# Kernel optimization log

Measured on AMD Instinct MI355X. Metric: run time of the kernel, lower is better.

## Reference

```python
import jax, jax.numpy as jnp
import numpy as np

N, F_IN, F_OUT = 8192, 1024, 512
ALPHA = 0.2   # LeakyReLU negative slope
C = 0.5       # RWR restart constant (hardcoded in original forward)


def setup_inputs() -> dict:
    key = jax.random.key(0)
    ks = jax.random.split(key, 9)
    x = jax.random.normal(ks[0], (N, F_IN), jnp.float32)
    adj = jax.random.normal(ks[1], (N, N), jnp.float32)  # additive attention bias
    adj_ad = jax.random.randint(ks[2], (N, N), 0, 20, jnp.int32)
    seq_W = jax.random.normal(ks[3], (F_OUT, F_IN), jnp.float32) / np.float32(np.sqrt(F_IN))
    f1_w = jax.random.normal(ks[4], (F_OUT,), jnp.float32) / np.float32(np.sqrt(F_OUT))
    f1_b = jax.random.normal(ks[5], (1,), jnp.float32)
    f2_w = jax.random.normal(ks[6], (F_OUT,), jnp.float32) / np.float32(np.sqrt(F_OUT))
    f2_b = jax.random.normal(ks[7], (1,), jnp.float32)
    bias = jnp.zeros((F_OUT,), jnp.float32)
    return {"x": x, "adj": adj, "adj_ad": adj_ad, "seq_W": seq_W,
            "f1_w": f1_w, "f1_b": f1_b, "f2_w": f2_w, "f2_b": f2_b, "bias": bias}


def _rwr(adj_ad):
    # Per-node random-walk-with-restart on a star graph over the selected
    # neighbors: solve (I - c*W) r = e0 where W is the (k_i+1)x(k_i+1) star
    # adjacency. Closed form of the per-node torch.inverse loop:
    #   r0 = 1 / (1 - c^2 k),  r_j = c / (1 - c^2 k)   (abs taken in original)
    # If (I - c*W) is singular the original falls back to rw_left = I - c*W,
    # giving r0 = 1, r_j = -c.
    k = jnp.sum((adj_ad > 1) & (adj_ad < 4), axis=1).astype(jnp.float32)  # [N]
    denom = 1.0 - (C * C) * k
    singular = denom == 0.0
    safe = jnp.where(singular, 1.0, denom)
    ri0 = jnp.where(singular, 1.0, jnp.abs(1.0 / safe))
    rin = jnp.where(singular, C, jnp.abs(C / safe))
    return jnp.stack([ri0, rin], axis=-1)  # [N, 2]: (center value, per-neighbor value)


def reference(x, adj, adj_ad, seq_W, f1_w, f1_b, f2_w, f2_b, bias):
    # conv1d(kernel=1) == linear: [N, F_IN] @ [F_IN, F_OUT]
    seq_fts = x @ seq_W.T                                  # [N, F_OUT]
    f1 = seq_fts @ f1_w + f1_b                             # [N]
    f2 = seq_fts @ f2_w + f2_b                             # [N]
    logits = f1[:, None] + f2[None, :]                     # [N, N]
    pre = jnp.where(logits > 0, logits, ALPHA * logits) + adj
    coefs = jax.nn.softmax(pre, axis=1)                    # dropout = identity (eval)
    h_prime = coefs @ seq_fts + bias                       # [N, F_OUT]
    h_prime = jax.nn.elu(h_prime)                          # concat=True
    ri = _rwr(adj_ad)
    return h_prime, ri
```

## Files before the change

kernel.cpp:

```cpp
#include <hip/hip_runtime.h>

#define NROWS 8192
#define FIN 1024
#define FOUT 512

typedef __attribute__((ext_vector_type(8))) short short8;
typedef __attribute__((ext_vector_type(4))) float f32x4;
typedef __attribute__((ext_vector_type(4))) unsigned short us4;

static __device__ __forceinline__ unsigned short f2bf(float f) {
  unsigned int u = __float_as_uint(f);
  u += 0x7fffu + ((u >> 16) & 1u);
  return (unsigned short)(u >> 16);
}
static __device__ __forceinline__ float bf2f(unsigned short h) {
  return __uint_as_float(((unsigned int)h) << 16);
}
static __device__ __forceinline__ void load_lds16(const void* g, void* l) {
  __builtin_amdgcn_global_load_lds((const __attribute__((address_space(1))) void*)g,
                                   (__attribute__((address_space(3))) void*)l, 16, 0, 0);
}

static __device__ __forceinline__ float dpp16_max(float x) {
  int t;
  t = __builtin_amdgcn_update_dpp(0, __float_as_int(x), 0xB1, 0xf, 0xf, true);
  x = fmaxf(x, __int_as_float(t));
  t = __builtin_amdgcn_update_dpp(0, __float_as_int(x), 0x4E, 0xf, 0xf, true);
  x = fmaxf(x, __int_as_float(t));
  t = __builtin_amdgcn_update_dpp(0, __float_as_int(x), 0x124, 0xf, 0xf, true);
  x = fmaxf(x, __int_as_float(t));
  t = __builtin_amdgcn_update_dpp(0, __float_as_int(x), 0x128, 0xf, 0xf, true);
  x = fmaxf(x, __int_as_float(t));
  return x;
}
static __device__ __forceinline__ float dpp16_add(float x) {
  int t;
  t = __builtin_amdgcn_update_dpp(0, __float_as_int(x), 0xB1, 0xf, 0xf, true);
  x += __int_as_float(t);
  t = __builtin_amdgcn_update_dpp(0, __float_as_int(x), 0x4E, 0xf, 0xf, true);
  x += __int_as_float(t);
  t = __builtin_amdgcn_update_dpp(0, __float_as_int(x), 0x124, 0xf, 0xf, true);
  x += __int_as_float(t);
  t = __builtin_amdgcn_update_dpp(0, __float_as_int(x), 0x128, 0xf, 0xf, true);
  x += __int_as_float(t);
  return x;
}

__global__ void k_split(const float* __restrict__ x, const float* __restrict__ w,
                        unsigned short* __restrict__ hi, unsigned short* __restrict__ lo) {
  long long base = ((long long)blockIdx.x * blockDim.x + threadIdx.x) * 4;
  const long long NX = (long long)NROWS * FIN;
  const float* src = (base < NX) ? (x + base) : (w + (base - NX));
  float4 v = *(const float4*)src;
  unsigned short h0 = f2bf(v.x), h1 = f2bf(v.y), h2 = f2bf(v.z), h3 = f2bf(v.w);
  us4 hv = {h0, h1, h2, h3};
  us4 lv = {f2bf(v.x - bf2f(h0)), f2bf(v.y - bf2f(h1)),
            f2bf(v.z - bf2f(h2)), f2bf(v.w - bf2f(h3))};
  *(us4*)(hi + base) = hv;
  *(us4*)(lo + base) = lv;
}

__global__ __launch_bounds__(256) void k_gemm1(const unsigned short* __restrict__ ah,
                                               const unsigned short* __restrict__ al,
                                               float* __restrict__ c) {
  __shared__ unsigned short sAh[128 * 32], sAl[128 * 32], sBh[64 * 32], sBl[64 * 32];
  const int tid = threadIdx.x;
  const int w = tid >> 6, l = tid & 63;
  const int bm = blockIdx.x >> 3, bn = blockIdx.x & 7;
  const int i0 = bm * 128, n0 = bn * 64;
  const unsigned short* bhp = ah + (long long)NROWS * FIN;
  const unsigned short* blp = al + (long long)NROWS * FIN;
  const int m_off = (w & 1) * 64, n_off = (w >> 1) * 32;
  const int lrow = l >> 2, lch = (l & 3) * 8;
  f32x4 acc[4][2] = {};
  for (int k0 = 0; k0 < FIN; k0 += 32) {
    __syncthreads();
    {
      int rA0 = w * 32, rA1 = w * 32 + 16, rB = w * 16;
      long long ga0 = (long long)(i0 + rA0 + lrow) * FIN + k0 + lch;
      long long ga1 = (long long)(i0 + rA1 + lrow) * FIN + k0 + lch;
      long long gb = (long long)(n0 + rB + lrow) * FIN + k0 + lch;
      load_lds16(ah + ga0, &sAh[rA0 * 32]);
      load_lds16(ah + ga1, &sAh[rA1 * 32]);
      load_lds16(al + ga0, &sAl[rA0 * 32]);
      load_lds16(al + ga1, &sAl[rA1 * 32]);
      load_lds16(bhp + gb, &sBh[rB * 32]);
      load_lds16(blp + gb, &sBl[rB * 32]);
    }
    __syncthreads();
    short8 a_h[4], a_l[4], b_h[2], b_l[2];
#pragma unroll
    for (int mi = 0; mi < 4; ++mi) {
      int off = (m_off + mi * 16 + (l & 15)) * 32 + (l >> 4) * 8;
      a_h[mi] = *(const short8*)&sAh[off];
      a_l[mi] = *(const short8*)&sAl[off];
    }
#pragma unroll
    for (int ni = 0; ni < 2; ++ni) {
      int off = (n_off + ni * 16 + (l & 15)) * 32 + (l >> 4) * 8;
      b_h[ni] = *(const short8*)&sBh[off];
      b_l[ni] = *(const short8*)&sBl[off];
    }
#pragma unroll
    for (int mi = 0; mi < 4; ++mi)
#pragma unroll
      for (int ni = 0; ni < 2; ++ni) {
        acc[mi][ni] = __builtin_amdgcn_mfma_f32_16x16x32_bf16(a_h[mi], b_h[ni], acc[mi][ni], 0, 0, 0);
        acc[mi][ni] = __builtin_amdgcn_mfma_f32_16x16x32_bf16(a_h[mi], b_l[ni], acc[mi][ni], 0, 0, 0);
        acc[mi][ni] = __builtin_amdgcn_mfma_f32_16x16x32_bf16(a_l[mi], b_h[ni], acc[mi][ni], 0, 0, 0);
      }
  }
#pragma unroll
  for (int mi = 0; mi < 4; ++mi)
#pragma unroll
    for (int ni = 0; ni < 2; ++ni)
#pragma unroll
      for (int rg = 0; rg < 4; ++rg) {
        int row = i0 + m_off + mi * 16 + (l >> 4) * 4 + rg;
        int col = n0 + n_off + ni * 16 + (l & 15);
        c[(long long)row * FOUT + col] = acc[mi][ni][rg];
      }
}

__global__ void k_f1f2(const float* __restrict__ sf, const float* __restrict__ f1w,
                       const float* __restrict__ f1b, const float* __restrict__ f2w,
                       const float* __restrict__ f2b, float* __restrict__ f1,
                       float* __restrict__ f2) {
  int w = threadIdx.x >> 6, l = threadIdx.x & 63;
  int i = blockIdx.x * 4 + w;
  const float* row = sf + (long long)i * FOUT;
  float4 v0 = *(const float4*)(row + l * 8);
  float4 v1 = *(const float4*)(row + l * 8 + 4);
  float4 a0 = *(const float4*)(f1w + l * 8);
  float4 a1 = *(const float4*)(f1w + l * 8 + 4);
  float4 b0 = *(const float4*)(f2w + l * 8);
  float4 b1 = *(const float4*)(f2w + l * 8 + 4);
  float s1 = v0.x * a0.x + v0.y * a0.y + v0.z * a0.z + v0.w * a0.w +
             v1.x * a1.x + v1.y * a1.y + v1.z * a1.z + v1.w * a1.w;
  float s2 = v0.x * b0.x + v0.y * b0.y + v0.z * b0.z + v0.w * b0.w +
             v1.x * b1.x + v1.y * b1.y + v1.z * b1.z + v1.w * b1.w;
#pragma unroll
  for (int m = 1; m < 64; m <<= 1) {
    s1 += __shfl_xor(s1, m, 64);
    s2 += __shfl_xor(s2, m, 64);
  }
  if (l == 0) {
    f1[i] = s1 + f1b[0];
    f2[i] = s2 + f2b[0];
  }
}

__global__ __launch_bounds__(256) void k_pack(const float* __restrict__ sf,
                                              unsigned short* __restrict__ vtp) {
  __shared__ unsigned short tile[32][33];
  const int t = threadIdx.x;
  const int k0 = blockIdx.x * 32;
  const int n0 = blockIdx.y * 32;
  {
    int kk = t >> 3, nq = (t & 7) * 4;
    float4 v = *(const float4*)(sf + (long long)(k0 + kk) * FOUT + n0 + nq);
    tile[kk][nq] = f2bf(v.x);
    tile[kk][nq + 1] = f2bf(v.y);
    tile[kk][nq + 2] = f2bf(v.z);
    tile[kk][nq + 3] = f2bf(v.w);
  }
  __syncthreads();
  int nt_loc = t >> 7, tt = t & 127;
  int lane = tt >> 1, jh = (tt & 1) * 4;
  int n_loc = nt_loc * 16 + (lane & 15);
  int k_loc = (lane >> 4) * 8 + jh;
  us4 u = {tile[k_loc][n_loc], tile[k_loc + 1][n_loc], tile[k_loc + 2][n_loc],
           tile[k_loc + 3][n_loc]};
  long long kt = blockIdx.x;
  long long nt = (long long)blockIdx.y * 2 + nt_loc;
  *(us4*)(vtp + ((kt * 32 + nt) * 64 + lane) * 8 + jh) = u;
}

__global__ __launch_bounds__(512) void k_flashp(const float* __restrict__ adj,
                                                const float* __restrict__ f1,
                                                const float* __restrict__ f2,
                                                const unsigned short* __restrict__ vtp,
                                                float* __restrict__ pacc,
                                                float* __restrict__ pstats) {
  __shared__ short p_sh[2][2][4][64][8];
  __shared__ float alpha_sh[2][32];
  const int tid = threadIdx.x, l = tid & 63, w = tid >> 6;
  const int rloc = tid >> 4, c16 = tid & 15;
  const int part = (blockIdx.x >> 2) & 1;
  const int rb = ((blockIdx.x >> 3) << 2) | (blockIdx.x & 3);
  const int r0 = rb * 32;
  const int jbase = part * 4096;
  const long long arow = (long long)(r0 + rloc) * NROWS;
  const float f1r = f1[r0 + rloc];
  const int nt_base = w * 4;
  const int mi_p = rloc >> 4;
  const int ks_p = c16 >> 2;
  const int lp = (rloc & 15) | ((c16 & 3) << 4);
  float m = -3.0e38f, lsum = 0.f;
  f32x4 acc[2][4] = {};
  float4 a0 = *(const float4*)(adj + arow + jbase + c16 * 8);
  float4 a1 = *(const float4*)(adj + arow + jbase + c16 * 8 + 4);
  float4 f20 = *(const float4*)(f2 + jbase + c16 * 8);
  float4 f21 = *(const float4*)(f2 + jbase + c16 * 8 + 4);
  for (int t = 0; t < 32; ++t) {
    const int j0 = jbase + t * 128;
    const int buf = t & 1;
    short8 vb[4][4];
    {
      const unsigned short* bb =
          vtp + (((long long)(j0 >> 5) * 32 + nt_base) * 64 + l) * 8;
#pragma unroll
      for (int ks = 0; ks < 4; ++ks)
#pragma unroll
        for (int ni = 0; ni < 4; ++ni)
          vb[ks][ni] = *(const short8*)(bb + ks * 16384 + ni * 512);
    }
    float z, p0, p1, p2, p3, p4, p5, p6, p7;
    z = f1r + f20.x; p0 = (z > 0.f ? z : 0.2f * z) + a0.x;
    z = f1r + f20.y; p1 = (z > 0.f ? z : 0.2f * z) + a0.y;
    z = f1r + f20.z; p2 = (z > 0.f ? z : 0.2f * z) + a0.z;
    z = f1r + f20.w; p3 = (z > 0.f ? z : 0.2f * z) + a0.w;
    z = f1r + f21.x; p4 = (z > 0.f ? z : 0.2f * z) + a1.x;
    z = f1r + f21.y; p5 = (z > 0.f ? z : 0.2f * z) + a1.y;
    z = f1r + f21.z; p6 = (z > 0.f ? z : 0.2f * z) + a1.z;
    z = f1r + f21.w; p7 = (z > 0.f ? z : 0.2f * z) + a1.w;
    float mt = fmaxf(fmaxf(fmaxf(p0, p1), fmaxf(p2, p3)), fmaxf(fmaxf(p4, p5), fmaxf(p6, p7)));
    mt = dpp16_max(mt);
    float m_new = fmaxf(m, mt);
    float al = __expf(m - m_new);
    p0 = __expf(p0 - m_new); p1 = __expf(p1 - m_new);
    p2 = __expf(p2 - m_new); p3 = __expf(p3 - m_new);
    p4 = __expf(p4 - m_new); p5 = __expf(p5 - m_new);
    p6 = __expf(p6 - m_new); p7 = __expf(p7 - m_new);
    float ps = p0 + p1 + p2 + p3 + p4 + p5 + p6 + p7;
    ps = dpp16_add(ps);
    lsum = lsum * al + ps;
    m = m_new;
    if (c16 == 0) alpha_sh[buf][rloc] = al;
    short8 pv;
    pv[0] = (short)f2bf(p0); pv[1] = (short)f2bf(p1);
    pv[2] = (short)f2bf(p2); pv[3] = (short)f2bf(p3);
    pv[4] = (short)f2bf(p4); pv[5] = (short)f2bf(p5);
    pv[6] = (short)f2bf(p6); pv[7] = (short)f2bf(p7);
    *(short8*)&p_sh[buf][mi_p][ks_p][lp][0] = pv;
    const int jn = (t < 31) ? j0 + 128 : j0;
    float4 na0 = *(const float4*)(adj + arow + jn + c16 * 8);
    float4 na1 = *(const float4*)(adj + arow + jn + c16 * 8 + 4);
    float4 nf20 = *(const float4*)(f2 + jn + c16 * 8);
    float4 nf21 = *(const float4*)(f2 + jn + c16 * 8 + 4);
    asm volatile("s_waitcnt lgkmcnt(0)" ::: "memory");
    __builtin_amdgcn_s_barrier();
    asm volatile("" ::: "memory");
    {
      f32x4 al0 = *(const f32x4*)&alpha_sh[buf][(l >> 4) * 4];
      f32x4 al1 = *(const f32x4*)&alpha_sh[buf][16 + (l >> 4) * 4];
#pragma unroll
      for (int ni = 0; ni < 4; ++ni)
#pragma unroll
        for (int rg = 0; rg < 4; ++rg) {
          acc[0][ni][rg] *= al0[rg];
          acc[1][ni][rg] *= al1[rg];
        }
    }
    __builtin_amdgcn_s_setprio(1);
#pragma unroll
    for (int ks = 0; ks < 4; ++ks) {
      short8 af0 = *(const short8*)&p_sh[buf][0][ks][l][0];
      short8 af1 = *(const short8*)&p_sh[buf][1][ks][l][0];
#pragma unroll
      for (int ni = 0; ni < 4; ++ni) {
        acc[0][ni] = __builtin_amdgcn_mfma_f32_16x16x32_bf16(af0, vb[ks][ni], acc[0][ni], 0, 0, 0);
        acc[1][ni] = __builtin_amdgcn_mfma_f32_16x16x32_bf16(af1, vb[ks][ni], acc[1][ni], 0, 0, 0);
      }
    }
    __builtin_amdgcn_s_setprio(0);
    a0 = na0; a1 = na1; f20 = nf20; f21 = nf21;
  }
  if (c16 == 0) {
    pstats[part * 2 * NROWS + (r0 + rloc)] = m;
    pstats[part * 2 * NROWS + NROWS + (r0 + rloc)] = lsum;
  }
  float* pc = pacc + (long long)part * NROWS * FOUT;
#pragma unroll
  for (int mi = 0; mi < 2; ++mi)
#pragma unroll
    for (int rg = 0; rg < 4; ++rg) {
      int row = mi * 16 + (l >> 4) * 4 + rg;
      long long gr = (long long)(r0 + row) * FOUT;
#pragma unroll
      for (int ni = 0; ni < 4; ++ni) {
        int col = w * 64 + ni * 16 + (l & 15);
        pc[gr + col] = acc[mi][ni][rg];
      }
    }
}

__global__ __launch_bounds__(512) void k_combine(const float* __restrict__ pacc,
                                                 const float* __restrict__ pstats,
                                                 const float* __restrict__ bias,
                                                 float* __restrict__ out) {
  const int tid = threadIdx.x;
  const int row = blockIdx.x * 4 + (tid >> 7);
  const int col = (tid & 127) * 4;
  const float m0 = pstats[row], l0 = pstats[NROWS + row];
  const float m1 = pstats[2 * NROWS + row], l1 = pstats[3 * NROWS + row];
  const float M = fmaxf(m0, m1);
  const float s0 = __expf(m0 - M), s1 = __expf(m1 - M);
  const float linv = 1.0f / (l0 * s0 + l1 * s1);
  float4 v0 = *(const float4*)(pacc + (long long)row * FOUT + col);
  float4 v1 = *(const float4*)(pacc + (long long)NROWS * FOUT + (long long)row * FOUT + col);
  float4 b = *(const float4*)(bias + col);
  float4 r;
  r.x = (v0.x * s0 + v1.x * s1) * linv + b.x;
  r.y = (v0.y * s0 + v1.y * s1) * linv + b.y;
  r.z = (v0.z * s0 + v1.z * s1) * linv + b.z;
  r.w = (v0.w * s0 + v1.w * s1) * linv + b.w;
  r.x = r.x > 0.f ? r.x : (__expf(r.x) - 1.f);
  r.y = r.y > 0.f ? r.y : (__expf(r.y) - 1.f);
  r.z = r.z > 0.f ? r.z : (__expf(r.z) - 1.f);
  r.w = r.w > 0.f ? r.w : (__expf(r.w) - 1.f);
  *(float4*)(out + (long long)row * FOUT + col) = r;
}

__global__ void k_rwr(const int* __restrict__ adj_ad, float* __restrict__ out) {
  __shared__ int ssum[4];
  const int tid = threadIdx.x, row = blockIdx.x;
  const long long base = (long long)row * NROWS;
  int cnt = 0;
#pragma unroll
  for (int k = 0; k < 8; ++k) {
    int4 v = *(const int4*)(adj_ad + base + ((long long)(k * 256 + tid)) * 4);
    cnt += (v.x > 1 && v.x < 4) + (v.y > 1 && v.y < 4) + (v.z > 1 && v.z < 4) + (v.w > 1 && v.w < 4);
  }
#pragma unroll
  for (int mws = 1; mws < 64; mws <<= 1) cnt += __shfl_xor(cnt, mws, 64);
  if ((tid & 63) == 0) ssum[tid >> 6] = cnt;
  __syncthreads();
  if (tid == 0) {
    float kk = (float)(ssum[0] + ssum[1] + ssum[2] + ssum[3]);
    float denom = 1.0f - 0.25f * kk;
    float r0, rn;
    if (denom == 0.0f) { r0 = 1.0f; rn = 0.5f; }
    else { r0 = fabsf(1.0f / denom); rn = fabsf(0.5f / denom); }
    out[(long long)NROWS * FOUT + row * 2] = r0;
    out[(long long)NROWS * FOUT + row * 2 + 1] = rn;
  }
}

extern "C" void kernel_launch(void* const* d_in, const int* in_sizes, int n_in,
                              void* d_out, int out_size, void* d_ws, size_t ws_size,
                              hipStream_t stream) {
  const float* x = (const float*)d_in[0];
  const float* adj = (const float*)d_in[1];
  const int* adj_ad = (const int*)d_in[2];
  const float* seqW = (const float*)d_in[3];
  const float* f1w = (const float*)d_in[4];
  const float* f1b = (const float*)d_in[5];
  const float* f2w = (const float*)d_in[6];
  const float* f2b = (const float*)d_in[7];
  const float* bias = (const float*)d_in[8];
  float* out = (float*)d_out;

  char* ws = (char*)d_ws;
  unsigned short* ah = (unsigned short*)ws;
  unsigned short* al = (unsigned short*)(ws + 17825792LL);
  float* sf = (float*)(ws + 35651584LL);
  unsigned short* vtp = (unsigned short*)(ws + 52428800LL);
  float* f1 = (float*)(ws + 60817408LL);
  float* f2 = (float*)(ws + 60850176LL);
  float* pacc = (float*)ws;
  float* pstats = (float*)(ws + 33554432LL);

  hipLaunchKernelGGL(k_split, dim3(8704), dim3(256), 0, stream, x, seqW, ah, al);
  hipLaunchKernelGGL(k_gemm1, dim3(512), dim3(256), 0, stream, ah, al, sf);
  hipLaunchKernelGGL(k_f1f2, dim3(2048), dim3(256), 0, stream, sf, f1w, f1b, f2w, f2b, f1, f2);
  hipLaunchKernelGGL(k_pack, dim3(256, 16), dim3(256), 0, stream, sf, vtp);
  hipLaunchKernelGGL(k_flashp, dim3(512), dim3(512), 0, stream, adj, f1, f2, vtp, pacc, pstats);
  hipLaunchKernelGGL(k_combine, dim3(2048), dim3(512), 0, stream, pacc, pstats, bias, out);
  hipLaunchKernelGGL(k_rwr, dim3(8192), dim3(256), 0, stream, adj_ad, out);
}
```

Measured before the change: 668.6 us.

## Double-buffer GEMM LDS tiles, hoist adj prefetch, use nontemporal streaming accesses

The projection GEMM now double-buffers its LDS tiles. It issues the next k-slice's global-to-LDS loads before computing on the current slice, which removes one barrier per iteration. In the attention kernel, the next tile's adj and f2 loads are issued earlier, before the softmax math, so their latency hides behind compute. Streaming accesses to adj, adj_ad, x/W and the partial accumulators are switched to nontemporal loads and stores to reduce cache pollution. The cost is double the LDS use in the GEMM, which could lower occupancy, and more live registers in the attention loop.

```diff
diff --git a/kernel.cpp b/kernel.cpp
--- a/kernel.cpp
+++ b/kernel.cpp
@@ -7,6 +7,7 @@
 typedef __attribute__((ext_vector_type(8))) short short8;
 typedef __attribute__((ext_vector_type(4))) float f32x4;
 typedef __attribute__((ext_vector_type(4))) unsigned short us4;
+typedef __attribute__((ext_vector_type(4))) int i32x4;
 
 static __device__ __forceinline__ unsigned short f2bf(float f) {
   unsigned int u = __float_as_uint(f);
@@ -51,11 +52,11 @@
   long long base = ((long long)blockIdx.x * blockDim.x + threadIdx.x) * 4;
   const long long NX = (long long)NROWS * FIN;
   const float* src = (base < NX) ? (x + base) : (w + (base - NX));
-  float4 v = *(const float4*)src;
-  unsigned short h0 = f2bf(v.x), h1 = f2bf(v.y), h2 = f2bf(v.z), h3 = f2bf(v.w);
+  f32x4 v = __builtin_nontemporal_load((const f32x4*)src);
+  unsigned short h0 = f2bf(v[0]), h1 = f2bf(v[1]), h2 = f2bf(v[2]), h3 = f2bf(v[3]);
   us4 hv = {h0, h1, h2, h3};
-  us4 lv = {f2bf(v.x - bf2f(h0)), f2bf(v.y - bf2f(h1)),
-            f2bf(v.z - bf2f(h2)), f2bf(v.w - bf2f(h3))};
+  us4 lv = {f2bf(v[0] - bf2f(h0)), f2bf(v[1] - bf2f(h1)),
+            f2bf(v[2] - bf2f(h2)), f2bf(v[3] - bf2f(h3))};
   *(us4*)(hi + base) = hv;
   *(us4*)(lo + base) = lv;
 }
@@ -63,7 +64,8 @@
 __global__ __launch_bounds__(256) void k_gemm1(const unsigned short* __restrict__ ah,
                                                const unsigned short* __restrict__ al,
                                                float* __restrict__ c) {
-  __shared__ unsigned short sAh[128 * 32], sAl[128 * 32], sBh[64 * 32], sBl[64 * 32];
+  __shared__ unsigned short sAh[2][128 * 32], sAl[2][128 * 32];
+  __shared__ unsigned short sBh[2][64 * 32], sBl[2][64 * 32];
   const int tid = threadIdx.x;
   const int w = tid >> 6, l = tid & 63;
   const int bm = blockIdx.x >> 3, bn = blockIdx.x & 7;
@@ -72,34 +74,38 @@
   const unsigned short* blp = al + (long long)NROWS * FIN;
   const int m_off = (w & 1) * 64, n_off = (w >> 1) * 32;
   const int lrow = l >> 2, lch = (l & 3) * 8;
+  const int rA0 = w * 32, rA1 = w * 32 + 16, rB = w * 16;
+
+  auto stage = [&](int kk, int b) {
+    long long ga0 = (long long)(i0 + rA0 + lrow) * FIN + kk + lch;
+    long long ga1 = (long long)(i0 + rA1 + lrow) * FIN + kk + lch;
+    long long gb = (long long)(n0 + rB + lrow) * FIN + kk + lch;
+    load_lds16(ah + ga0, &sAh[b][rA0 * 32]);
+    load_lds16(ah + ga1, &sAh[b][rA1 * 32]);
+    load_lds16(al + ga0, &sAl[b][rA0 * 32]);
+    load_lds16(al + ga1, &sAl[b][rA1 * 32]);
+    load_lds16(bhp + gb, &sBh[b][rB * 32]);
+    load_lds16(blp + gb, &sBl[b][rB * 32]);
+  };
+
   f32x4 acc[4][2] = {};
+  stage(0, 0);
   for (int k0 = 0; k0 < FIN; k0 += 32) {
+    const int cur = (k0 >> 5) & 1;
     __syncthreads();
-    {
-      int rA0 = w * 32, rA1 = w * 32 + 16, rB = w * 16;
-      long long ga0 = (long long)(i0 + rA0 + lrow) * FIN + k0 + lch;
-      long long ga1 = (long long)(i0 + rA1 + lrow) * FIN + k0 + lch;
-      long long gb = (long long)(n0 + rB + lrow) * FIN + k0 + lch;
-      load_lds16(ah + ga0, &sAh[rA0 * 32]);
-      load_lds16(ah + ga1, &sAh[rA1 * 32]);
-      load_lds16(al + ga0, &sAl[rA0 * 32]);
-      load_lds16(al + ga1, &sAl[rA1 * 32]);
-      load_lds16(bhp + gb, &sBh[rB * 32]);
-      load_lds16(blp + gb, &sBl[rB * 32]);
-    }
-    __syncthreads();
+    if (k0 + 32 < FIN) stage(k0 + 32, cur ^ 1);
     short8 a_h[4], a_l[4], b_h[2], b_l[2];
 #pragma unroll
     for (int mi = 0; mi < 4; ++mi) {
       int off = (m_off + mi * 16 + (l & 15)) * 32 + (l >> 4) * 8;
-      a_h[mi] = *(const short8*)&sAh[off];
-      a_l[mi] = *(const short8*)&sAl[off];
+      a_h[mi] = *(const short8*)&sAh[cur][off];
+      a_l[mi] = *(const short8*)&sAl[cur][off];
     }
 #pragma unroll
     for (int ni = 0; ni < 2; ++ni) {
       int off = (n_off + ni * 16 + (l & 15)) * 32 + (l >> 4) * 8;
-      b_h[ni] = *(const short8*)&sBh[off];
-      b_l[ni] = *(const short8*)&sBl[off];
+      b_h[ni] = *(const short8*)&sBh[cur][off];
+      b_l[ni] = *(const short8*)&sBl[cur][off];
     }
 #pragma unroll
     for (int mi = 0; mi < 4; ++mi)
@@ -198,8 +204,8 @@
   const int lp = (rloc & 15) | ((c16 & 3) << 4);
   float m = -3.0e38f, lsum = 0.f;
   f32x4 acc[2][4] = {};
-  float4 a0 = *(const float4*)(adj + arow + jbase + c16 * 8);
-  float4 a1 = *(const float4*)(adj + arow + jbase + c16 * 8 + 4);
+  f32x4 a0 = __builtin_nontemporal_load((const f32x4*)(adj + arow + jbase + c16 * 8));
+  f32x4 a1 = __builtin_nontemporal_load((const f32x4*)(adj + arow + jbase + c16 * 8 + 4));
   float4 f20 = *(const float4*)(f2 + jbase + c16 * 8);
   float4 f21 = *(const float4*)(f2 + jbase + c16 * 8 + 4);
   for (int t = 0; t < 32; ++t) {
@@ -215,15 +221,20 @@
         for (int ni = 0; ni < 4; ++ni)
           vb[ks][ni] = *(const short8*)(bb + ks * 16384 + ni * 512);
     }
+    const int jn = (t < 31) ? j0 + 128 : j0;
+    f32x4 na0 = __builtin_nontemporal_load((const f32x4*)(adj + arow + jn + c16 * 8));
+    f32x4 na1 = __builtin_nontemporal_load((const f32x4*)(adj + arow + jn + c16 * 8 + 4));
+    float4 nf20 = *(const float4*)(f2 + jn + c16 * 8);
+    float4 nf21 = *(const float4*)(f2 + jn + c16 * 8 + 4);
     float z, p0, p1, p2, p3, p4, p5, p6, p7;
-    z = f1r + f20.x; p0 = (z > 0.f ? z : 0.2f * z) + a0.x;
-    z = f1r + f20.y; p1 = (z > 0.f ? z : 0.2f * z) + a0.y;
-    z = f1r + f20.z; p2 = (z > 0.f ? z : 0.2f * z) + a0.z;
-    z = f1r + f20.w; p3 = (z > 0.f ? z : 0.2f * z) + a0.w;
-    z = f1r + f21.x; p4 = (z > 0.f ? z : 0.2f * z) + a1.x;
-    z = f1r + f21.y; p5 = (z > 0.f ? z : 0.2f * z) + a1.y;
-    z = f1r + f21.z; p6 = (z > 0.f ? z : 0.2f * z) + a1.z;
-    z = f1r + f21.w; p7 = (z > 0.f ? z : 0.2f * z) + a1.w;
+    z = f1r + f20.x; p0 = (z > 0.f ? z : 0.2f * z) + a0[0];
+    z = f1r + f20.y; p1 = (z > 0.f ? z : 0.2f * z) + a0[1];
+    z = f1r + f20.z; p2 = (z > 0.f ? z : 0.2f * z) + a0[2];
+    z = f1r + f20.w; p3 = (z > 0.f ? z : 0.2f * z) + a0[3];
+    z = f1r + f21.x; p4 = (z > 0.f ? z : 0.2f * z) + a1[0];
+    z = f1r + f21.y; p5 = (z > 0.f ? z : 0.2f * z) + a1[1];
+    z = f1r + f21.z; p6 = (z > 0.f ? z : 0.2f * z) + a1[2];
+    z = f1r + f21.w; p7 = (z > 0.f ? z : 0.2f * z) + a1[3];
     float mt = fmaxf(fmaxf(fmaxf(p0, p1), fmaxf(p2, p3)), fmaxf(fmaxf(p4, p5), fmaxf(p6, p7)));
     mt = dpp16_max(mt);
     float m_new = fmaxf(m, mt);
@@ -243,11 +254,6 @@
     pv[4] = (short)f2bf(p4); pv[5] = (short)f2bf(p5);
     pv[6] = (short)f2bf(p6); pv[7] = (short)f2bf(p7);
     *(short8*)&p_sh[buf][mi_p][ks_p][lp][0] = pv;
-    const int jn = (t < 31) ? j0 + 128 : j0;
-    float4 na0 = *(const float4*)(adj + arow + jn + c16 * 8);
-    float4 na1 = *(const float4*)(adj + arow + jn + c16 * 8 + 4);
-    float4 nf20 = *(const float4*)(f2 + jn + c16 * 8);
-    float4 nf21 = *(const float4*)(f2 + jn + c16 * 8 + 4);
     asm volatile("s_waitcnt lgkmcnt(0)" ::: "memory");
     __builtin_amdgcn_s_barrier();
     asm volatile("" ::: "memory");
@@ -290,7 +296,7 @@
 #pragma unroll
       for (int ni = 0; ni < 4; ++ni) {
         int col = w * 64 + ni * 16 + (l & 15);
-        pc[gr + col] = acc[mi][ni][rg];
+        __builtin_nontemporal_store(acc[mi][ni][rg], pc + gr + col);
       }
     }
 }
@@ -307,14 +313,15 @@
   const float M = fmaxf(m0, m1);
   const float s0 = __expf(m0 - M), s1 = __expf(m1 - M);
   const float linv = 1.0f / (l0 * s0 + l1 * s1);
-  float4 v0 = *(const float4*)(pacc + (long long)row * FOUT + col);
-  float4 v1 = *(const float4*)(pacc + (long long)NROWS * FOUT + (long long)row * FOUT + col);
+  f32x4 v0 = __builtin_nontemporal_load((const f32x4*)(pacc + (long long)row * FOUT + col));
+  f32x4 v1 = __builtin_nontemporal_load(
+      (const f32x4*)(pacc + (long long)NROWS * FOUT + (long long)row * FOUT + col));
   float4 b = *(const float4*)(bias + col);
   float4 r;
-  r.x = (v0.x * s0 + v1.x * s1) * linv + b.x;
-  r.y = (v0.y * s0 + v1.y * s1) * linv + b.y;
-  r.z = (v0.z * s0 + v1.z * s1) * linv + b.z;
-  r.w = (v0.w * s0 + v1.w * s1) * linv + b.w;
+  r.x = (v0[0] * s0 + v1[0] * s1) * linv + b.x;
+  r.y = (v0[1] * s0 + v1[1] * s1) * linv + b.y;
+  r.z = (v0[2] * s0 + v1[2] * s1) * linv + b.z;
+  r.w = (v0[3] * s0 + v1[3] * s1) * linv + b.w;
   r.x = r.x > 0.f ? r.x : (__expf(r.x) - 1.f);
   r.y = r.y > 0.f ? r.y : (__expf(r.y) - 1.f);
   r.z = r.z > 0.f ? r.z : (__expf(r.z) - 1.f);
@@ -329,8 +336,10 @@
   int cnt = 0;
 #pragma unroll
   for (int k = 0; k < 8; ++k) {
-    int4 v = *(const int4*)(adj_ad + base + ((long long)(k * 256 + tid)) * 4);
-    cnt += (v.x > 1 && v.x < 4) + (v.y > 1 && v.y < 4) + (v.z > 1 && v.z < 4) + (v.w > 1 && v.w < 4);
+    i32x4 v = __builtin_nontemporal_load(
+        (const i32x4*)(adj_ad + base + ((long long)(k * 256 + tid)) * 4));
+    cnt += (v[0] > 1 && v[0] < 4) + (v[1] > 1 && v[1] < 4) +
+           (v[2] > 1 && v[2] < 4) + (v[3] > 1 && v[3] < 4);
   }
 #pragma unroll
   for (int mws = 1; mws < 64; mws <<= 1) cnt += __shfl_xor(cnt, mws, 64);
```

New measurement: 678.1 us. About the same (+1.4%).
